# Performance work log

Measured on AMD Instinct MI355X. Metric: run time of the kernel, lower is better.

## Reference

```python
import jax, jax.numpy as jnp
import numpy as np

BS, SEQ, H = 64, 512, 768
E, T, K = 32, 64, 64


def setup_inputs() -> dict:
    key = jax.random.key(0)
    ks = jax.random.split(key, 16)
    return {
        "hidden_states": jax.random.normal(ks[0], (BS, SEQ, H), dtype=jnp.float32),
        "Wsrc": jax.random.normal(ks[1], (862, 384), dtype=jnp.float32) * 0.02,
        "Wtgt": jax.random.normal(ks[2], (862, 384), dtype=jnp.float32) * 0.02,
        "W_cls": jax.random.normal(ks[3], (2, 6144), dtype=jnp.float32) * 0.02,
        "b_cls": jnp.zeros((2,), dtype=jnp.float32),
        "W_topic": jax.random.normal(ks[4], (2, 6144), dtype=jnp.float32) * 0.02,
        "b_topic": jnp.zeros((2,), dtype=jnp.float32),
        "W_token": jax.random.normal(ks[5], (2, 6144), dtype=jnp.float32) * 0.02,
        "b_token": jnp.zeros((2,), dtype=jnp.float32),
        "source_ids": jax.random.randint(ks[6], (BS,), 0, 862),
        "target_ids": jax.random.randint(ks[7], (BS,), 0, 862),
        "ent_inds": jax.random.randint(ks[8], (BS, E), 0, SEQ - 1),
        "ent_mask": jnp.ones((BS, E), dtype=jnp.float32),
        "topic_inds": jax.random.randint(ks[9], (BS, T), 0, SEQ),
        "topic_mask": jnp.ones((BS, T), dtype=jnp.float32),
        "token_inds": jax.random.randint(ks[10], (BS, K), 0, SEQ),
        "token_mask": jnp.ones((BS, K), dtype=jnp.float32),
    }


def reference(hidden_states, Wsrc, Wtgt, W_cls, b_cls, W_topic, b_topic,
              W_token, b_token, source_ids, target_ids, ent_inds, ent_mask,
              topic_inds, topic_mask, token_inds, token_mask):
    bs = hidden_states.shape[0]
    # domain embedding: concat(source_emb, target_emb) -> [bs, 768] -> [bs, 96, 8]
    domain = jnp.concatenate([Wsrc[source_ids], Wtgt[target_ids]], axis=1)
    d0 = domain.reshape(bs, 96, 8)

    def gather(inds, mask, offset=0):
        # ragged gather of hidden states at token positions, zero-padded slots masked
        h = jnp.take_along_axis(hidden_states, (inds + offset)[:, :, None], axis=1)
        return h * mask[:, :, None]  # [bs, L, 768]

    ent_h = gather(ent_inds, ent_mask, offset=1)
    topic_h = gather(topic_inds, topic_mask)
    token_h = gather(token_inds, token_mask)

    # CLS bilinear: outer product over the 8-dim factor, [bs,96,8,8] -> [bs,6144]
    cls_h = hidden_states[:, 0, :].reshape(bs, 96, 8)
    bl_cls = (d0[:, :, :, None] * cls_h[:, :, None, :]).reshape(bs, 6144)
    cls_logits = jax.nn.softmax(bl_cls @ W_cls.T + b_cls, axis=1)

    def bilin(h, W, b):
        h4 = h.reshape(bs, -1, 96, 8)  # [bs, L, 96, 8]
        bl = (d0[:, None, :, :, None] * h4[:, :, :, None, :]).reshape(bs, h4.shape[1], 6144)
        return bl @ W.T + b  # [bs, L, n_out]

    topic_logits = jax.nn.softmax(bilin(topic_h, W_topic, b_topic), axis=2)
    token_logits = bilin(token_h, W_token, b_token)
    return cls_logits, topic_logits, token_logits
```

## Files before the change

kernel.cpp:

```cpp
#include <hip/hip_runtime.h>

#define BSZ 64
#define SEQ 512
#define HD  768
#define TT  64
#define SL  8
#define WPB 4

__global__ __launch_bounds__(256) void fused_bilinear_kernel(
    const float* __restrict__ hidden,
    const float* __restrict__ Wsrc,
    const float* __restrict__ Wtgt,
    const float* __restrict__ W_cls,
    const float* __restrict__ b_cls,
    const float* __restrict__ W_topic,
    const float* __restrict__ b_topic,
    const float* __restrict__ W_token,
    const float* __restrict__ b_token,
    const int*   __restrict__ source_ids,
    const int*   __restrict__ target_ids,
    const int*   __restrict__ topic_inds,
    const float* __restrict__ topic_mask,
    const int*   __restrict__ token_inds,
    const float* __restrict__ token_mask,
    float*       __restrict__ out)
{
    __shared__ __align__(16) float dom[HD];
    __shared__ __align__(16) float V[3 * 2 * HD];

    const int b     = blockIdx.x / SL;
    const int slice = blockIdx.x % SL;
    const int tid   = threadIdx.x;

    const int sid = source_ids[b];
    const int tgt = target_ids[b];
    for (int j = tid; j < HD; j += 256) {
        dom[j] = (j < 384) ? Wsrc[sid * 384 + j] : Wtgt[tgt * 384 + (j - 384)];
    }
    __syncthreads();

    const float* Ws[3] = {W_cls, W_topic, W_token};
    for (int w = 0; w < 3; ++w) {
        const float* Wp = Ws[w];
        for (int o = 0; o < 2; ++o) {
            for (int d = tid; d < HD; d += 256) {
                const int m = d >> 3, c = d & 7;
                const float* wrow = Wp + o * 6144 + m * 64 + c;
                float acc = 0.f;
                #pragma unroll
                for (int a = 0; a < 8; ++a)
                    acc = fmaf(dom[m * 8 + a], wrow[a * 8], acc);
                V[(w * 2 + o) * HD + d] = acc;
            }
        }
    }
    __syncthreads();

    const int wave = tid >> 6;
    const int lane = tid & 63;

    for (int t = slice * WPB + wave; t < 129; t += SL * WPB) {
        int w, pos, outoff;
        float mask;
        const float* bias;
        bool do_softmax;
        if (t == 0) {
            w = 0; pos = 0; mask = 1.f; bias = b_cls; do_softmax = true;
            outoff = b * 2;
        } else if (t <= 64) {
            const int l = t - 1;
            w = 1; pos = topic_inds[b * TT + l]; mask = topic_mask[b * TT + l];
            bias = b_topic; do_softmax = true;
            outoff = 128 + (b * TT + l) * 2;
        } else {
            const int l = t - 65;
            w = 2; pos = token_inds[b * TT + l]; mask = token_mask[b * TT + l];
            bias = b_token; do_softmax = false;
            outoff = 128 + BSZ * TT * 2 + (b * TT + l) * 2;
        }

        const float4* hrow = reinterpret_cast<const float4*>(
            hidden + ((size_t)b * SEQ + (size_t)pos) * HD);
        const float4* v0 = reinterpret_cast<const float4*>(&V[(w * 2 + 0) * HD]);
        const float4* v1 = reinterpret_cast<const float4*>(&V[(w * 2 + 1) * HD]);

        float a0 = 0.f, a1 = 0.f;
        #pragma unroll
        for (int k = 0; k < 3; ++k) {
            const float4 h4 = hrow[lane + k * 64];
            const float4 x0 = v0[lane + k * 64];
            const float4 x1 = v1[lane + k * 64];
            a0 = fmaf(h4.x, x0.x, a0); a0 = fmaf(h4.y, x0.y, a0);
            a0 = fmaf(h4.z, x0.z, a0); a0 = fmaf(h4.w, x0.w, a0);
            a1 = fmaf(h4.x, x1.x, a1); a1 = fmaf(h4.y, x1.y, a1);
            a1 = fmaf(h4.z, x1.z, a1); a1 = fmaf(h4.w, x1.w, a1);
        }
        #pragma unroll
        for (int off = 32; off > 0; off >>= 1) {
            a0 += __shfl_down(a0, off, 64);
            a1 += __shfl_down(a1, off, 64);
        }

        if (lane == 0) {
            const float l0 = fmaf(mask, a0, bias[0]);
            const float l1 = fmaf(mask, a1, bias[1]);
            if (do_softmax) {
                const float mx = fmaxf(l0, l1);
                const float e0 = __expf(l0 - mx);
                const float e1 = __expf(l1 - mx);
                const float inv = 1.f / (e0 + e1);
                out[outoff]     = e0 * inv;
                out[outoff + 1] = e1 * inv;
            } else {
                out[outoff]     = l0;
                out[outoff + 1] = l1;
            }
        }
    }
}

extern "C" void kernel_launch(void* const* d_in, const int* in_sizes, int n_in,
                              void* d_out, int out_size, void* d_ws, size_t ws_size,
                              hipStream_t stream) {
    const float* hidden     = (const float*)d_in[0];
    const float* Wsrc       = (const float*)d_in[1];
    const float* Wtgt       = (const float*)d_in[2];
    const float* W_cls      = (const float*)d_in[3];
    const float* b_cls      = (const float*)d_in[4];
    const float* W_topic    = (const float*)d_in[5];
    const float* b_topic    = (const float*)d_in[6];
    const float* W_token    = (const float*)d_in[7];
    const float* b_token    = (const float*)d_in[8];
    const int*   source_ids = (const int*)d_in[9];
    const int*   target_ids = (const int*)d_in[10];
    const int*   topic_inds = (const int*)d_in[13];
    const float* topic_mask = (const float*)d_in[14];
    const int*   token_inds = (const int*)d_in[15];
    const float* token_mask = (const float*)d_in[16];
    float* out = (float*)d_out;

    fused_bilinear_kernel<<<BSZ * SL, 256, 0, stream>>>(
        hidden, Wsrc, Wtgt, W_cls, b_cls, W_topic, b_topic, W_token, b_token,
        source_ids, target_ids, topic_inds, topic_mask, token_inds, token_mask, out);
}
```

Before: 170.0 us.

## Split V precompute into separate kernel and give each task its own wavefront

Replaces the single fused kernel, in which each of 8 slices per batch recomputed the per-batch V vectors in shared memory, with two launches. The first computes V once per batch into workspace; the second assigns one wavefront per (batch, task) pair and reads V from global memory. This removes the eightfold redundant V computation and the serial task loop, at the cost of an extra launch and global-memory round trip for V.

```diff
diff --git a/kernel.cpp b/kernel.cpp
--- a/kernel.cpp
+++ b/kernel.cpp
@@ -4,117 +4,117 @@
 #define SEQ 512
 #define HD  768
 #define TT  64
-#define SL  8
-#define WPB 4
+#define NROW 6
+#define NTASK 129
 
-__global__ __launch_bounds__(256) void fused_bilinear_kernel(
-    const float* __restrict__ hidden,
+__global__ __launch_bounds__(256) void compute_V_kernel(
     const float* __restrict__ Wsrc,
     const float* __restrict__ Wtgt,
     const float* __restrict__ W_cls,
-    const float* __restrict__ b_cls,
     const float* __restrict__ W_topic,
-    const float* __restrict__ b_topic,
     const float* __restrict__ W_token,
-    const float* __restrict__ b_token,
     const int*   __restrict__ source_ids,
     const int*   __restrict__ target_ids,
+    float*       __restrict__ Vg)
+{
+    __shared__ __align__(16) float dom[HD];
+    const int b   = blockIdx.x;
+    const int tid = threadIdx.x;
+
+    const int sid = source_ids[b];
+    const int tgt = target_ids[b];
+    for (int j = tid; j < HD; j += 256)
+        dom[j] = (j < 384) ? Wsrc[sid * 384 + j] : Wtgt[tgt * 384 + (j - 384)];
+    __syncthreads();
+
+    for (int idx = tid; idx < NROW * HD; idx += 256) {
+        const int r = idx / HD;
+        const int d = idx - r * HD;
+        const int w = r >> 1, o = r & 1;
+        const float* Wp = (w == 0) ? W_cls : (w == 1) ? W_topic : W_token;
+        const int m = d >> 3, c = d & 7;
+        const float* wrow = Wp + o * 6144 + m * 64 + c;
+        float acc = 0.f;
+        #pragma unroll
+        for (int a = 0; a < 8; ++a)
+            acc = fmaf(dom[m * 8 + a], wrow[a * 8], acc);
+        Vg[(size_t)b * (NROW * HD) + idx] = acc;
+    }
+}
+
+__global__ __launch_bounds__(256) void task_kernel(
+    const float* __restrict__ hidden,
+    const float* __restrict__ Vg,
+    const float* __restrict__ b_cls,
+    const float* __restrict__ b_topic,
+    const float* __restrict__ b_token,
     const int*   __restrict__ topic_inds,
     const float* __restrict__ topic_mask,
     const int*   __restrict__ token_inds,
     const float* __restrict__ token_mask,
     float*       __restrict__ out)
 {
-    __shared__ __align__(16) float dom[HD];
-    __shared__ __align__(16) float V[3 * 2 * HD];
+    const int wg   = blockIdx.x * 4 + (threadIdx.x >> 6);
+    const int lane = threadIdx.x & 63;
+    const int b    = wg / NTASK;
+    const int t    = wg - b * NTASK;
 
-    const int b     = blockIdx.x / SL;
-    const int slice = blockIdx.x % SL;
-    const int tid   = threadIdx.x;
+    int w, pos, outoff;
+    float mask;
+    const float* bias;
+    bool do_softmax;
+    if (t == 0) {
+        w = 0; pos = 0; mask = 1.f; bias = b_cls; do_softmax = true;
+        outoff = b * 2;
+    } else if (t <= TT) {
+        const int l = t - 1;
+        w = 1; pos = topic_inds[b * TT + l]; mask = topic_mask[b * TT + l];
+        bias = b_topic; do_softmax = true;
+        outoff = 128 + (b * TT + l) * 2;
+    } else {
+        const int l = t - 1 - TT;
+        w = 2; pos = token_inds[b * TT + l]; mask = token_mask[b * TT + l];
+        bias = b_token; do_softmax = false;
+        outoff = 128 + BSZ * TT * 2 + (b * TT + l) * 2;
+    }
 
-    const int sid = source_ids[b];
-    const int tgt = target_ids[b];
-    for (int j = tid; j < HD; j += 256) {
-        dom[j] = (j < 384) ? Wsrc[sid * 384 + j] : Wtgt[tgt * 384 + (j - 384)];
+    const float4* hrow = reinterpret_cast<const float4*>(
+        hidden + ((size_t)b * SEQ + (size_t)pos) * HD);
+    const float4* v0 = reinterpret_cast<const float4*>(
+        Vg + ((size_t)b * NROW + w * 2 + 0) * HD);
+    const float4* v1 = reinterpret_cast<const float4*>(
+        Vg + ((size_t)b * NROW + w * 2 + 1) * HD);
+
+    float a0 = 0.f, a1 = 0.f;
+    #pragma unroll
+    for (int k = 0; k < 3; ++k) {
+        const float4 h4 = hrow[lane + k * 64];
+        const float4 x0 = v0[lane + k * 64];
+        const float4 x1 = v1[lane + k * 64];
+        a0 = fmaf(h4.x, x0.x, a0); a1 = fmaf(h4.x, x1.x, a1);
+        a0 = fmaf(h4.y, x0.y, a0); a1 = fmaf(h4.y, x1.y, a1);
+        a0 = fmaf(h4.z, x0.z, a0); a1 = fmaf(h4.z, x1.z, a1);
+        a0 = fmaf(h4.w, x0.w, a0); a1 = fmaf(h4.w, x1.w, a1);
     }
-    __syncthreads();
+    #pragma unroll
+    for (int off = 32; off > 0; off >>= 1) {
+        a0 += __shfl_down(a0, off, 64);
+        a1 += __shfl_down(a1, off, 64);
+    }
 
-    const float* Ws[3] = {W_cls, W_topic, W_token};
-    for (int w = 0; w < 3; ++w) {
-        const float* Wp = Ws[w];
-        for (int o = 0; o < 2; ++o) {
-            for (int d = tid; d < HD; d += 256) {
-                const int m = d >> 3, c = d & 7;
-                const float* wrow = Wp + o * 6144 + m * 64 + c;
-                float acc = 0.f;
-                #pragma unroll
-                for (int a = 0; a < 8; ++a)
-                    acc = fmaf(dom[m * 8 + a], wrow[a * 8], acc);
-                V[(w * 2 + o) * HD + d] = acc;
-            }
-        }
-    }
-    __syncthreads();
-
-    const int wave = tid >> 6;
-    const int lane = tid & 63;
-
-    for (int t = slice * WPB + wave; t < 129; t += SL * WPB) {
-        int w, pos, outoff;
-        float mask;
-        const float* bias;
-        bool do_softmax;
-        if (t == 0) {
-            w = 0; pos = 0; mask = 1.f; bias = b_cls; do_softmax = true;
-            outoff = b * 2;
-        } else if (t <= 64) {
-            const int l = t - 1;
-            w = 1; pos = topic_inds[b * TT + l]; mask = topic_mask[b * TT + l];
-            bias = b_topic; do_softmax = true;
-            outoff = 128 + (b * TT + l) * 2;
+    if (lane == 0) {
+        const float l0 = fmaf(mask, a0, bias[0]);
+        const float l1 = fmaf(mask, a1, bias[1]);
+        if (do_softmax) {
+            const float mx = fmaxf(l0, l1);
+            const float e0 = __expf(l0 - mx);
+            const float e1 = __expf(l1 - mx);
+            const float inv = 1.f / (e0 + e1);
+            out[outoff]     = e0 * inv;
+            out[outoff + 1] = e1 * inv;
         } else {
-            const int l = t - 65;
-            w = 2; pos = token_inds[b * TT + l]; mask = token_mask[b * TT + l];
-            bias = b_token; do_softmax = false;
-            outoff = 128 + BSZ * TT * 2 + (b * TT + l) * 2;
-        }
-
-        const float4* hrow = reinterpret_cast<const float4*>(
-            hidden + ((size_t)b * SEQ + (size_t)pos) * HD);
-        const float4* v0 = reinterpret_cast<const float4*>(&V[(w * 2 + 0) * HD]);
-        const float4* v1 = reinterpret_cast<const float4*>(&V[(w * 2 + 1) * HD]);
-
-        float a0 = 0.f, a1 = 0.f;
-        #pragma unroll
-        for (int k = 0; k < 3; ++k) {
-            const float4 h4 = hrow[lane + k * 64];
-            const float4 x0 = v0[lane + k * 64];
-            const float4 x1 = v1[lane + k * 64];
-            a0 = fmaf(h4.x, x0.x, a0); a0 = fmaf(h4.y, x0.y, a0);
-            a0 = fmaf(h4.z, x0.z, a0); a0 = fmaf(h4.w, x0.w, a0);
-            a1 = fmaf(h4.x, x1.x, a1); a1 = fmaf(h4.y, x1.y, a1);
-            a1 = fmaf(h4.z, x1.z, a1); a1 = fmaf(h4.w, x1.w, a1);
-        }
-        #pragma unroll
-        for (int off = 32; off > 0; off >>= 1) {
-            a0 += __shfl_down(a0, off, 64);
-            a1 += __shfl_down(a1, off, 64);
-        }
-
-        if (lane == 0) {
-            const float l0 = fmaf(mask, a0, bias[0]);
-            const float l1 = fmaf(mask, a1, bias[1]);
-            if (do_softmax) {
-                const float mx = fmaxf(l0, l1);
-                const float e0 = __expf(l0 - mx);
-                const float e1 = __expf(l1 - mx);
-                const float inv = 1.f / (e0 + e1);
-                out[outoff]     = e0 * inv;
-                out[outoff + 1] = e1 * inv;
-            } else {
-                out[outoff]     = l0;
-                out[outoff + 1] = l1;
-            }
+            out[outoff]     = l0;
+            out[outoff + 1] = l1;
         }
     }
 }
@@ -138,8 +138,12 @@
     const int*   token_inds = (const int*)d_in[15];
     const float* token_mask = (const float*)d_in[16];
     float* out = (float*)d_out;
+    float* Vg  = (float*)d_ws;
 
-    fused_bilinear_kernel<<<BSZ * SL, 256, 0, stream>>>(
-        hidden, Wsrc, Wtgt, W_cls, b_cls, W_topic, b_topic, W_token, b_token,
-        source_ids, target_ids, topic_inds, topic_mask, token_inds, token_mask, out);
+    compute_V_kernel<<<BSZ, 256, 0, stream>>>(
+        Wsrc, Wtgt, W_cls, W_topic, W_token, source_ids, target_ids, Vg);
+
+    task_kernel<<<(BSZ * NTASK) / 4, 256, 0, stream>>>(
+        hidden, Vg, b_cls, b_topic, b_token,
+        topic_inds, topic_mask, token_inds, token_mask, out);
 }
```

After: 165.7 us. -2.5%, faster.
